# Optimization experiments

Measured on AMD Instinct MI355X. Metric: run time of the kernel, lower is better.

## Reference

```python
import jax, jax.numpy as jnp
import numpy as np

TAU = 0.4
EPS = 1e-8


def setup_inputs() -> dict:
    key = jax.random.key(0)
    k1, k2 = jax.random.split(key)
    B, N, C, M = 4, 4096, 256, 2048
    l_feat = jax.random.normal(k1, (B, N, C), dtype=jnp.float32)
    g_feat = jax.random.normal(k2, (B, C, M), dtype=jnp.float32)
    return {"l_feat": l_feat, "g_feat": g_feat}


def reference(l_feat, g_feat):
    # l_feat: [B, N, C], g_feat: [B, C, M]
    # cosine similarity over channel dim C (torch CosineSimilarity, dim=2)
    l_norm = jnp.linalg.norm(l_feat, axis=2)          # [B, N]
    g_norm = jnp.linalg.norm(g_feat, axis=1)          # [B, M]
    dot = jnp.einsum('bnc,bcm->bnm', l_feat, g_feat)  # [B, N, M]
    cos_sim = dot / jnp.maximum(l_norm[:, :, None] * g_norm[:, None, :], EPS)
    sim = jnp.exp(cos_sim / TAU)                      # [B, N, M]
    # diag_embed(rowsum) followed by linalg.inv and bmm is exactly
    # row-wise division by the degree (row sum)
    sim = sim / jnp.sum(sim, axis=2, keepdims=True)
    # bmm(sim, g_feat^T): [B,N,M] x [B,M,C] -> [B,N,C]
    g_enh = jnp.einsum('bnm,bcm->bnc', sim, g_feat)
    return l_feat + g_enh
```

## Files before the change

### kernel.cpp

```cpp
#include <hip/hip_runtime.h>

#define B_ 4
#define N_ 4096
#define C_ 256
#define M_ 2048

typedef __attribute__((ext_vector_type(8))) short short8;
typedef __attribute__((ext_vector_type(4))) float f32x4;

union U16x8 { uint4 u4; unsigned short us[8]; short8 s8; };
union U16x4 { uint2 u2; unsigned short us[4]; };

__device__ __forceinline__ float bf2f(unsigned short h) {
    unsigned int u = ((unsigned int)h) << 16;
    return __builtin_bit_cast(float, u);
}
__device__ __forceinline__ unsigned short f2bf(float f) {
    unsigned int u = __builtin_bit_cast(unsigned int, f);
    u += 0x7FFFu + ((u >> 16) & 1u);
    return (unsigned short)(u >> 16);
}

#define GLB_AS(p) ((const __attribute__((address_space(1))) unsigned int*)(p))
#define LDS_AS(p) ((__attribute__((address_space(3))) unsigned int*)(p))

__global__ __launch_bounds__(1024) void k_prep(const float* __restrict__ g,
                                               unsigned short* __restrict__ gcm3,
                                               unsigned short* __restrict__ gmc) {
    __shared__ float red[16][64];
    __shared__ float sInv[64];
    __shared__ unsigned short T[64 * 66];
    const int t = blockIdx.x;
    const int b = blockIdx.y, m0 = t * 64;
    const int tid = threadIdx.x;
    const int ml = tid & 63, cq = tid >> 6;

    const float* gb = g + (size_t)b * C_ * M_ + m0 + ml;
    float ss = 0.f;
#pragma unroll 4
    for (int i = 0; i < 16; ++i) {
        float v = gb[(size_t)(cq * 16 + i) * M_];
        ss += v * v;
    }
    red[cq][ml] = ss;
    __syncthreads();
    if (cq == 0) {
        float t0 = 0.f;
#pragma unroll
        for (int k = 0; k < 16; ++k) t0 += red[k][ml];
        sInv[ml] = 1.f / fmaxf(sqrtf(t0), 1e-8f);
    }
    __syncthreads();

    unsigned short* gmcb = gmc + ((size_t)b * M_ + m0) * C_;
    unsigned short* gcm3b = gcm3 + (size_t)b * 524288 +
                            (size_t)(t >> 1) * 32768 + (t & 1) * 4;

    for (int c0 = 0; c0 < C_; c0 += 64) {
        const float* gbase = g + ((size_t)b * C_ + c0) * M_ + m0;
        {
            int ci = tid >> 4, mq = (tid & 15) * 4;
            float4 v = *(const float4*)(gbase + (size_t)ci * M_ + mq);
            uint2 pk;
            pk.x = (unsigned)f2bf(v.x) | ((unsigned)f2bf(v.y) << 16);
            pk.y = (unsigned)f2bf(v.z) | ((unsigned)f2bf(v.w) << 16);
            const int cg = c0 + ci;
            const int kh = mq >> 4, kq = (mq >> 2) & 3;
            *(uint2*)(gcm3b + kh * 8192 + (cg >> 4) * 512 + kq * 128 +
                      (cg & 15) * 8) = pk;
            T[ci * 66 + mq + 0] = f2bf(v.x * sInv[mq + 0]);
            T[ci * 66 + mq + 1] = f2bf(v.y * sInv[mq + 1]);
            T[ci * 66 + mq + 2] = f2bf(v.z * sInv[mq + 2]);
            T[ci * 66 + mq + 3] = f2bf(v.w * sInv[mq + 3]);
        }
        __syncthreads();
        if (tid < 512) {
            int mr = tid >> 3, cc8 = (tid & 7) * 8;
            U16x8 t8;
#pragma unroll
            for (int k = 0; k < 8; ++k) t8.us[k] = T[(cc8 + k) * 66 + mr];
            *(uint4*)(gmcb + (size_t)mr * C_ + c0 + cc8) = t8.u4;
        }
        __syncthreads();
    }
}

__global__ __launch_bounds__(512, 1) void k_main(
    const float* __restrict__ l,
    const unsigned short* __restrict__ gcm3,
    const unsigned short* __restrict__ gmc,
    float* __restrict__ out)
{
    __shared__ __align__(16) char sMem[132096];
    unsigned short* sGmcD = (unsigned short*)sMem;
    unsigned short* sGcm3 = (unsigned short*)(sMem + 65536);
    float (*sDen)[64] = (float (*)[64])(sMem + 131072);

    const int tid = threadIdx.x;
    const int w = tid >> 6;
    const int lane = tid & 63;
    const int l15 = lane & 15;
    const int quad = lane >> 4;
    const int kh = w & 3;
    const int rh = w >> 2;

    const int bid = blockIdx.x;
    const int xcd = bid & 7;
    const int b = xcd >> 1;
    const int row0 = (((bid >> 3) << 1) | (xcd & 1)) * 64;

    int goffA[4];
#pragma unroll
    for (int i = 0; i < 4; ++i) {
        int p = (w * 4 + i) * 64 + lane;
        int rA = p >> 5;
        goffA[i] = rA * 256 + (((p & 31) ^ (rA & 31)) << 3);
    }

    const unsigned short* gmc_b = gmc + (size_t)b * M_ * C_;
    const unsigned short* gcm3_b = gcm3 + (size_t)b * 524288;

    auto dmaA = [&](int tile, int reg) {
#pragma unroll
        for (int i = 0; i < 4; ++i)
            __builtin_amdgcn_global_load_lds(GLB_AS(gmc_b + (size_t)tile * 16384 + goffA[i]),
                                             LDS_AS(&sGmcD[reg * 16384 + (w * 4 + i) * 512]), 16, 0, 0);
    };
    auto dmaB = [&](int pair) {
#pragma unroll
        for (int i = 0; i < 8; ++i)
            __builtin_amdgcn_global_load_lds(GLB_AS(gcm3_b + (size_t)pair * 32768 + (w * 8 + i) * 512 + lane * 8),
                                             LDS_AS(&sGcm3[(w * 8 + i) * 512]), 16, 0, 0);
    };

    dmaA(0, 0);
    dmaA(1, 1);
    dmaB(0);

    short8 qf[2][8];
#pragma unroll
    for (int rt = 0; rt < 2; ++rt) {
        const float* lrow = l + ((size_t)b * N_ + row0 + rh * 32 + rt * 16 + l15) * C_;
        U16x8 qt[8];
        float ss = 0.f;
#pragma unroll
        for (int kk = 0; kk < 8; ++kk) {
            float4 x0 = *(const float4*)(lrow + kk * 32 + quad * 8);
            float4 x1 = *(const float4*)(lrow + kk * 32 + quad * 8 + 4);
            ss += x0.x*x0.x + x0.y*x0.y + x0.z*x0.z + x0.w*x0.w;
            ss += x1.x*x1.x + x1.y*x1.y + x1.z*x1.z + x1.w*x1.w;
            qt[kk].us[0] = f2bf(x0.x); qt[kk].us[1] = f2bf(x0.y);
            qt[kk].us[2] = f2bf(x0.z); qt[kk].us[3] = f2bf(x0.w);
            qt[kk].us[4] = f2bf(x1.x); qt[kk].us[5] = f2bf(x1.y);
            qt[kk].us[6] = f2bf(x1.z); qt[kk].us[7] = f2bf(x1.w);
        }
        ss += __shfl_xor(ss, 16);
        ss += __shfl_xor(ss, 32);
        const float invl = 1.0f / fmaxf(sqrtf(ss), 1e-8f);
#pragma unroll
        for (int kk = 0; kk < 8; ++kk) {
            U16x8 t;
#pragma unroll
            for (int j = 0; j < 8; ++j) t.us[j] = f2bf(bf2f(qt[kk].us[j]) * invl);
            qf[rt][kk] = t.s8;
        }
    }

    __syncthreads();

    f32x4 zero = {0.f, 0.f, 0.f, 0.f};
    f32x4 o[2][16];
#pragma unroll
    for (int i = 0; i < 2; ++i)
#pragma unroll
        for (int j = 0; j < 16; ++j) o[i][j] = zero;
    float dl0 = 0.f, dl1 = 0.f;

    const unsigned short* gAbase = &sGmcD[(kh * 16 + l15) * 256];
    const int rxor = (kh * 16 + l15) & 31;
    const unsigned short* gB3 = &sGcm3[kh * 8192 + quad * 128 + l15 * 8];

    for (int p = 0; p < 16; ++p) {
        U16x4 pkE0, pkE1, pkO0, pkO1;

        {
            f32x4 sa0 = zero, sa1 = zero;
#pragma unroll
            for (int kk = 0; kk < 8; ++kk) {
                short8 ag = *(const short8*)&gAbase[((kk * 4 + quad) ^ rxor) << 3];
                sa0 = __builtin_amdgcn_mfma_f32_16x16x32_bf16(ag, qf[0][kk], sa0, 0, 0, 0);
                sa1 = __builtin_amdgcn_mfma_f32_16x16x32_bf16(ag, qf[1][kk], sa1, 0, 0, 0);
            }
#pragma unroll
            for (int r = 0; r < 4; ++r) {
                float p0 = exp2f(sa0[r] * 3.6067376022224085f);
                float p1 = exp2f(sa1[r] * 3.6067376022224085f);
                dl0 += p0; dl1 += p1;
                pkE0.us[r] = f2bf(p0);
                pkE1.us[r] = f2bf(p1);
            }
        }
        {
            f32x4 sa0 = zero, sa1 = zero;
#pragma unroll
            for (int kk = 0; kk < 8; ++kk) {
                short8 ag = *(const short8*)&gAbase[16384 + (((kk * 4 + quad) ^ rxor) << 3)];
                sa0 = __builtin_amdgcn_mfma_f32_16x16x32_bf16(ag, qf[0][kk], sa0, 0, 0, 0);
                sa1 = __builtin_amdgcn_mfma_f32_16x16x32_bf16(ag, qf[1][kk], sa1, 0, 0, 0);
            }
#pragma unroll
            for (int r = 0; r < 4; ++r) {
                float p0 = exp2f(sa0[r] * 3.6067376022224085f);
                float p1 = exp2f(sa1[r] * 3.6067376022224085f);
                dl0 += p0; dl1 += p1;
                pkO0.us[r] = f2bf(p0);
                pkO1.us[r] = f2bf(p1);
            }
        }

        __syncthreads();
        if (p < 15) { dmaA(2 * p + 2, 0); dmaA(2 * p + 3, 1); }

        U16x8 ap0, ap1;
#pragma unroll
        for (int r = 0; r < 4; ++r) {
            ap0.us[r] = pkE0.us[r]; ap0.us[4 + r] = pkO0.us[r];
            ap1.us[r] = pkE1.us[r]; ap1.us[4 + r] = pkO1.us[r];
        }
#pragma unroll
        for (int ct = 0; ct < 16; ++ct) {
            U16x8 bb;
            bb.u4 = *(const uint4*)&gB3[ct * 512];
            o[0][ct] = __builtin_amdgcn_mfma_f32_16x16x32_bf16(ap0.s8, bb.s8, o[0][ct], 0, 0, 0);
            o[1][ct] = __builtin_amdgcn_mfma_f32_16x16x32_bf16(ap1.s8, bb.s8, o[1][ct], 0, 0, 0);
        }

        __syncthreads();
        if (p < 15) dmaB(p + 1);
    }

    {
        float d0 = dl0;
        d0 += __shfl_xor(d0, 16);
        d0 += __shfl_xor(d0, 32);
        float d1 = dl1;
        d1 += __shfl_xor(d1, 16);
        d1 += __shfl_xor(d1, 32);
        if (quad == 0) {
            sDen[kh][rh * 32 + l15] = d0;
            sDen[kh][rh * 32 + 16 + l15] = d1;
        }
    }

    f32x4* red4 = (f32x4*)sMem;
    const int wslot = kh * 1024 + quad * 16 + l15;
    const int rslot = (4 * kh) * 64 + quad * 16 + l15;
    f32x4 oacc0[4], oacc1[4];

#define RED_ROUND(RH, OSRC, ODST)                                              \
    __syncthreads();                                                           \
    if (rh == (RH)) {                                                          \
        _Pragma("unroll")                                                      \
        for (int j = 0; j < 16; ++j) red4[wslot + j * 64] = OSRC[j];           \
    }                                                                          \
    __syncthreads();                                                           \
    if (rh == (RH)) {                                                          \
        _Pragma("unroll")                                                      \
        for (int jj = 0; jj < 4; ++jj) {                                       \
            const int base = rslot + jj * 64;                                  \
            ODST[jj] = red4[base] + red4[base + 1024] +                        \
                       red4[base + 2048] + red4[base + 3072];                  \
        }                                                                      \
    }

    RED_ROUND(0, o[0], oacc0)
    RED_ROUND(0, o[1], oacc1)
    RED_ROUND(1, o[0], oacc0)
    RED_ROUND(1, o[1], oacc1)
#undef RED_ROUND

    const float* lb = l + ((size_t)b * N_ + row0 + rh * 32) * C_;
    float* ob = out + ((size_t)b * N_ + row0 + rh * 32) * C_;
#pragma unroll
    for (int r = 0; r < 4; ++r) {
        {
            const int row = quad * 4 + r;
            const int grow = rh * 32 + row;
            const float inv = 1.f / (sDen[0][grow] + sDen[1][grow] + sDen[2][grow] + sDen[3][grow]);
            const size_t rb = (size_t)row * C_;
#pragma unroll
            for (int jj = 0; jj < 4; ++jj) {
                const int c = kh * 64 + jj * 16 + l15;
                ob[rb + c] = lb[rb + c] + oacc0[jj][r] * inv;
            }
        }
        {
            const int row = 16 + quad * 4 + r;
            const int grow = rh * 32 + row;
            const float inv = 1.f / (sDen[0][grow] + sDen[1][grow] + sDen[2][grow] + sDen[3][grow]);
            const size_t rb = (size_t)row * C_;
#pragma unroll
            for (int jj = 0; jj < 4; ++jj) {
                const int c = kh * 64 + jj * 16 + l15;
                ob[rb + c] = lb[rb + c] + oacc1[jj][r] * inv;
            }
        }
    }
}

extern "C" void kernel_launch(void* const* d_in, const int* in_sizes, int n_in,
                              void* d_out, int out_size, void* d_ws, size_t ws_size,
                              hipStream_t stream) {
    (void)in_sizes; (void)n_in; (void)out_size; (void)ws_size;
    const float* l = (const float*)d_in[0];
    const float* g = (const float*)d_in[1];
    float* outp = (float*)d_out;

    char* ws = (char*)d_ws;
    unsigned short* gmc = (unsigned short*)ws;
    unsigned short* gcm3 = (unsigned short*)(ws + (size_t)B_ * M_ * C_ * 2);

    k_prep<<<dim3(M_ / 64, B_), 1024, 0, stream>>>(g, gcm3, gmc);
    k_main<<<dim3(N_ / 64 * B_), 512, 0, stream>>>(l, gcm3, gmc, outp);
}
```

Measured before the change: 138.9 us.

## Fuse prep and main kernels into one cooperative launch with grid sync

Merges the g-feature normalization/bf16 conversion kernel into the main kernel. Each of 256 blocks does a half-channel slice of the prep work, then the grid synchronizes with a cooperative-groups barrier before the main attention/GEMM phase. This removes a separate kernel launch and the gap between the two kernels. In exchange it adds a grid-wide barrier, and the column-norm reduction is computed twice, once per channel-half block. It also depends on all 256 blocks being co-resident, which the cooperative launch requires.

Result: slower. 211.8 us (+52.5%).

```diff
diff --git a/kernel.cpp b/kernel.cpp
--- a/kernel.cpp
+++ b/kernel.cpp
@@ -1,4 +1,7 @@
 #include <hip/hip_runtime.h>
+#include <hip/hip_cooperative_groups.h>
+
+namespace cg = cooperative_groups;
 
 #define B_ 4
 #define N_ 4096
@@ -24,79 +27,89 @@
 #define GLB_AS(p) ((const __attribute__((address_space(1))) unsigned int*)(p))
 #define LDS_AS(p) ((__attribute__((address_space(3))) unsigned int*)(p))
 
-__global__ __launch_bounds__(1024) void k_prep(const float* __restrict__ g,
-                                               unsigned short* __restrict__ gcm3,
-                                               unsigned short* __restrict__ gmc) {
-    __shared__ float red[16][64];
-    __shared__ float sInv[64];
-    __shared__ unsigned short T[64 * 66];
-    const int t = blockIdx.x;
-    const int b = blockIdx.y, m0 = t * 64;
-    const int tid = threadIdx.x;
-    const int ml = tid & 63, cq = tid >> 6;
-
-    const float* gb = g + (size_t)b * C_ * M_ + m0 + ml;
-    float ss = 0.f;
-#pragma unroll 4
-    for (int i = 0; i < 16; ++i) {
-        float v = gb[(size_t)(cq * 16 + i) * M_];
-        ss += v * v;
-    }
-    red[cq][ml] = ss;
-    __syncthreads();
-    if (cq == 0) {
-        float t0 = 0.f;
-#pragma unroll
-        for (int k = 0; k < 16; ++k) t0 += red[k][ml];
-        sInv[ml] = 1.f / fmaxf(sqrtf(t0), 1e-8f);
-    }
-    __syncthreads();
-
-    unsigned short* gmcb = gmc + ((size_t)b * M_ + m0) * C_;
-    unsigned short* gcm3b = gcm3 + (size_t)b * 524288 +
-                            (size_t)(t >> 1) * 32768 + (t & 1) * 4;
-
-    for (int c0 = 0; c0 < C_; c0 += 64) {
-        const float* gbase = g + ((size_t)b * C_ + c0) * M_ + m0;
-        {
-            int ci = tid >> 4, mq = (tid & 15) * 4;
-            float4 v = *(const float4*)(gbase + (size_t)ci * M_ + mq);
-            uint2 pk;
-            pk.x = (unsigned)f2bf(v.x) | ((unsigned)f2bf(v.y) << 16);
-            pk.y = (unsigned)f2bf(v.z) | ((unsigned)f2bf(v.w) << 16);
-            const int cg = c0 + ci;
-            const int kh = mq >> 4, kq = (mq >> 2) & 3;
-            *(uint2*)(gcm3b + kh * 8192 + (cg >> 4) * 512 + kq * 128 +
-                      (cg & 15) * 8) = pk;
-            T[ci * 66 + mq + 0] = f2bf(v.x * sInv[mq + 0]);
-            T[ci * 66 + mq + 1] = f2bf(v.y * sInv[mq + 1]);
-            T[ci * 66 + mq + 2] = f2bf(v.z * sInv[mq + 2]);
-            T[ci * 66 + mq + 3] = f2bf(v.w * sInv[mq + 3]);
-        }
-        __syncthreads();
-        if (tid < 512) {
-            int mr = tid >> 3, cc8 = (tid & 7) * 8;
-            U16x8 t8;
-#pragma unroll
-            for (int k = 0; k < 8; ++k) t8.us[k] = T[(cc8 + k) * 66 + mr];
-            *(uint4*)(gmcb + (size_t)mr * C_ + c0 + cc8) = t8.u4;
-        }
-        __syncthreads();
-    }
-}
-
-__global__ __launch_bounds__(512, 1) void k_main(
+__global__ __launch_bounds__(512, 1) void k_fused(
     const float* __restrict__ l,
-    const unsigned short* __restrict__ gcm3,
-    const unsigned short* __restrict__ gmc,
+    const float* __restrict__ g,
+    unsigned short* __restrict__ gcm3,
+    unsigned short* __restrict__ gmc,
     float* __restrict__ out)
 {
     __shared__ __align__(16) char sMem[132096];
+
+    const int tid = threadIdx.x;
+    const int bid = blockIdx.x;
+
+    {
+        float (*red)[64] = (float (*)[64])sMem;
+        float* sInv = (float*)(sMem + 2048);
+        unsigned short* T = (unsigned short*)(sMem + 2304);
+
+        const int unit = bid >> 1;
+        const int t = unit & 31;
+        const int b = unit >> 5;
+        const int ch = bid & 1;
+        const int m0 = t * 64;
+        const int ml = tid & 63, cq = tid >> 6;
+
+        const float* gb = g + (size_t)b * C_ * M_ + m0 + ml;
+        float ss = 0.f;
+#pragma unroll 4
+        for (int i = 0; i < 32; ++i) {
+            float v = gb[(size_t)(cq * 32 + i) * M_];
+            ss += v * v;
+        }
+        red[cq][ml] = ss;
+        __syncthreads();
+        if (cq == 0) {
+            float t0 = 0.f;
+#pragma unroll
+            for (int k = 0; k < 8; ++k) t0 += red[k][ml];
+            sInv[ml] = 1.f / fmaxf(sqrtf(t0), 1e-8f);
+        }
+        __syncthreads();
+
+        unsigned short* gmcb = gmc + ((size_t)b * M_ + m0) * C_;
+        unsigned short* gcm3b = gcm3 + (size_t)b * 524288 +
+                                (size_t)(t >> 1) * 32768 + (t & 1) * 4;
+
+        for (int c0 = ch * 128; c0 < ch * 128 + 128; c0 += 64) {
+            const float* gbase = g + ((size_t)b * C_ + c0) * M_ + m0;
+#pragma unroll
+            for (int j = 0; j < 2; ++j) {
+                int id = tid + 512 * j;
+                int ci = id >> 4, mq = (id & 15) * 4;
+                float4 v = *(const float4*)(gbase + (size_t)ci * M_ + mq);
+                uint2 pk;
+                pk.x = (unsigned)f2bf(v.x) | ((unsigned)f2bf(v.y) << 16);
+                pk.y = (unsigned)f2bf(v.z) | ((unsigned)f2bf(v.w) << 16);
+                const int cg = c0 + ci;
+                const int kh = mq >> 4, kq = (mq >> 2) & 3;
+                *(uint2*)(gcm3b + kh * 8192 + (cg >> 4) * 512 + kq * 128 +
+                          (cg & 15) * 8) = pk;
+                T[ci * 66 + mq + 0] = f2bf(v.x * sInv[mq + 0]);
+                T[ci * 66 + mq + 1] = f2bf(v.y * sInv[mq + 1]);
+                T[ci * 66 + mq + 2] = f2bf(v.z * sInv[mq + 2]);
+                T[ci * 66 + mq + 3] = f2bf(v.w * sInv[mq + 3]);
+            }
+            __syncthreads();
+            {
+                int mr = tid >> 3, cc8 = (tid & 7) * 8;
+                U16x8 t8;
+#pragma unroll
+                for (int k = 0; k < 8; ++k) t8.us[k] = T[(cc8 + k) * 66 + mr];
+                *(uint4*)(gmcb + (size_t)mr * C_ + c0 + cc8) = t8.u4;
+            }
+            __syncthreads();
+        }
+    }
+
+    __threadfence();
+    cg::this_grid().sync();
+
     unsigned short* sGmcD = (unsigned short*)sMem;
     unsigned short* sGcm3 = (unsigned short*)(sMem + 65536);
     float (*sDen)[64] = (float (*)[64])(sMem + 131072);
 
-    const int tid = threadIdx.x;
     const int w = tid >> 6;
     const int lane = tid & 63;
     const int l15 = lane & 15;
@@ -104,7 +117,6 @@
     const int kh = w & 3;
     const int rh = w >> 2;
 
-    const int bid = blockIdx.x;
     const int xcd = bid & 7;
     const int b = xcd >> 1;
     const int row0 = (((bid >> 3) << 1) | (xcd & 1)) * 64;
@@ -320,6 +332,7 @@
     unsigned short* gmc = (unsigned short*)ws;
     unsigned short* gcm3 = (unsigned short*)(ws + (size_t)B_ * M_ * C_ * 2);
 
-    k_prep<<<dim3(M_ / 64, B_), 1024, 0, stream>>>(g, gcm3, gmc);
-    k_main<<<dim3(N_ / 64 * B_), 512, 0, stream>>>(l, gcm3, gmc, outp);
+    void* args[] = {(void*)&l, (void*)&g, (void*)&gcm3, (void*)&gmc, (void*)&outp};
+    hipLaunchCooperativeKernel((const void*)k_fused, dim3(256), dim3(512),
+                               args, 0, stream);
 }
```
